# Kernel optimization log

Measured on AMD Instinct MI355X. Metric: run time of the kernel, lower is better.

## Reference

```python
import jax, jax.numpy as jnp
import numpy as np
from jax import lax

GUARD_CELLS = 80
BG_CELLS = 80
ALPHA = 1.8
CFAR_UNITS = 1 + 2 * GUARD_CELLS + 2 * BG_CELLS          # 321
GUARD_UNITS = 2 * GUARD_CELLS + 1                         # 161
BG_AREA = CFAR_UNITS ** 2 - GUARD_UNITS ** 2              # background ring cell count
FRONT_DIV = (GUARD_UNITS ** 2) * ALPHA


def box_sum(x, k):
    """Same-padded KxK box sum over NCHW x (C=1), via separable 1D convs.

    Mathematically identical to a Conv2d with all-ones KxK kernel, zero bias,
    padding (k-1)//2 -- but O(N*K) instead of O(N*K^2).
    """
    p = (k - 1) // 2
    kh = jnp.ones((1, 1, k, 1), x.dtype)  # OIHW
    kw = jnp.ones((1, 1, 1, k), x.dtype)
    y = lax.conv_general_dilated(x, kh, window_strides=(1, 1), padding=[(p, p), (0, 0)])
    y = lax.conv_general_dilated(y, kw, window_strides=(1, 1), padding=[(0, 0), (p, p)])
    return y


def setup_inputs() -> dict:
    key = jax.random.key(0)
    x = jax.random.uniform(key, (4, 1, 1024, 1024), dtype=jnp.float32)
    return {"x": x}


def reference(x) -> jnp.ndarray:
    allsum = box_sum(x, CFAR_UNITS)            # conv1: 321x321 ones box
    front = box_sum(x, GUARD_UNITS)            # conv2: 161x161 ones box
    back = (allsum - front) / jnp.float32(BG_AREA)     # div1: 1x1 conv = scale
    front = front / jnp.float32(FRONT_DIV)             # div2: 1x1 conv = scale
    return front / back
```

## Files before the change

kernel.cpp:

```cpp
#include <hip/hip_runtime.h>
#include <hip/hip_bf16.h>


#define IMG 4
#define H 1024
#define W 1024
#define SEGR 4
#define NSEG 256
#define PADL 164
#define PADR 164
#define ROWLEN (PADL + W + PADR)

__global__ __launch_bounds__(256) void hbv_kernel(const float* __restrict__ x,
                                                  float* __restrict__ g161,
                                                  float* __restrict__ g321,
                                                  float* __restrict__ Btot) {
    __shared__ float P[4][ROWLEN];
    const int wave = threadIdx.x >> 6;
    const int lane = threadIdx.x & 63;
    const int tid  = threadIdx.x;
    const int blk  = blockIdx.x;
    const size_t rowbase = (size_t)blk << 2;

    {
        const size_t row = rowbase + wave;
        const float4* xr = reinterpret_cast<const float4*>(x + row * W);
        float v[16];
        float4 a0 = xr[(lane << 2) + 0];
        float4 a1 = xr[(lane << 2) + 1];
        float4 a2 = xr[(lane << 2) + 2];
        float4 a3 = xr[(lane << 2) + 3];
        v[0]=a0.x; v[1]=a0.y; v[2]=a0.z; v[3]=a0.w;
        v[4]=a1.x; v[5]=a1.y; v[6]=a1.z; v[7]=a1.w;
        v[8]=a2.x; v[9]=a2.y; v[10]=a2.z; v[11]=a2.w;
        v[12]=a3.x; v[13]=a3.y; v[14]=a3.z; v[15]=a3.w;
        float s = 0.f;
#pragma unroll
        for (int j = 0; j < 16; ++j) { s += v[j]; v[j] = s; }
        float t = s;
#pragma unroll
        for (int d = 1; d < 64; d <<= 1) {
            float u = __shfl_up(t, d, 64);
            if (lane >= d) t += u;
        }
        const float off = t - s;
#pragma unroll
        for (int j = 0; j < 16; ++j) v[j] += off;
        const float tot = __shfl(t, 63, 64);

        float* rowP = P[wave];
        float4* Pr = reinterpret_cast<float4*>(rowP + PADL);
        Pr[(lane << 2) + 0] = make_float4(v[0], v[1], v[2], v[3]);
        Pr[(lane << 2) + 1] = make_float4(v[4], v[5], v[6], v[7]);
        Pr[(lane << 2) + 2] = make_float4(v[8], v[9], v[10], v[11]);
        Pr[(lane << 2) + 3] = make_float4(v[12], v[13], v[14], v[15]);
        float4* Pz = reinterpret_cast<float4*>(rowP);
        if (lane < 41) {
            Pz[lane]       = make_float4(0.f, 0.f, 0.f, 0.f);
            Pz[297 + lane] = make_float4(tot, tot, tot, tot);
        }
    }
    __syncthreads();

    float acc1[4] = {0.f, 0.f, 0.f, 0.f};
    float acc3[4] = {0.f, 0.f, 0.f, 0.f};
#pragma unroll
    for (int rr = 0; rr < SEGR; ++rr) {
        const float* Pr = &P[rr][PADL];
        float* o1 = g161 + (rowbase + rr) * W;
        float* o3 = g321 + (rowbase + rr) * W;
#pragma unroll
        for (int j = 0; j < 4; ++j) {
            const int c = tid + (j << 8);
            acc1[j] += Pr[c + 80]  - Pr[c - 81];
            acc3[j] += Pr[c + 160] - Pr[c - 161];
            o1[c] = acc1[j];
            o3[c] = acc3[j];
        }
    }

    const int img = blk >> 8;
    const int seg = blk & 255;
    float* bt1 = Btot + ((size_t)img << 18)         + ((size_t)seg << 10);
    float* bt3 = Btot + ((size_t)(IMG + img) << 18) + ((size_t)seg << 10);
#pragma unroll
    for (int j = 0; j < 4; ++j) {
        bt1[tid + (j << 8)] = acc1[j];
        bt3[tid + (j << 8)] = acc3[j];
    }
}

__global__ __launch_bounds__(256) void segscan_kernel(float* __restrict__ Btot) {
    __shared__ float T[4][64];
    const int wave = threadIdx.x >> 6;
    const int lane = threadIdx.x & 63;
    const int bi   = blockIdx.x >> 4;
    const int col  = ((blockIdx.x & 15) << 6) + lane;
    const size_t base = ((size_t)bi << 18) + ((size_t)(wave << 6) << 10) + col;

    float v[64];
#pragma unroll
    for (int s = 0; s < 64; ++s) v[s] = Btot[base + ((size_t)s << 10)];
    float run = 0.f;
#pragma unroll
    for (int s = 0; s < 64; ++s) { const float t = v[s]; v[s] = run; run += t; }
    T[wave][lane] = run;
    __syncthreads();
    float off = 0.f;
    for (int w = 0; w < wave; ++w) off += T[w][lane];
#pragma unroll
    for (int s = 0; s < 64; ++s) Btot[base + ((size_t)s << 10)] = v[s] + off;
}

__global__ __launch_bounds__(512) void final_kernel(const float* __restrict__ g161,
                                                    const float* __restrict__ g321,
                                                    const float* __restrict__ SP,
                                                    float* __restrict__ out) {
    const int img = blockIdx.x >> 9;
    const int r   = ((blockIdx.x & 511) << 1) + (threadIdx.x >> 8);
    const int c4  = threadIdx.x & 255;

    const float4* P1 = reinterpret_cast<const float4*>(g161 + ((size_t)img << 20));
    const float4* P3 = reinterpret_cast<const float4*>(g321 + ((size_t)img << 20));
    const float4* SP1 = reinterpret_cast<const float4*>(SP) + ((size_t)img << 16);
    const float4* SP3 = reinterpret_cast<const float4*>(SP) + ((size_t)(IMG + img) << 16);

    const int hi1 = min(r + 80, H - 1),  lo1 = r - 81;
    const int hi3 = min(r + 160, H - 1), lo3 = r - 161;

    float4 f  = P1[((size_t)hi1 << 8) + c4];
    float4 fs = SP1[(((size_t)hi1 >> 2) << 8) + c4];
    float fx = f.x + fs.x, fy = f.y + fs.y, fz = f.z + fs.z, fw = f.w + fs.w;
    if (lo1 >= 0) {
        float4 g  = P1[((size_t)lo1 << 8) + c4];
        float4 gs = SP1[(((size_t)lo1 >> 2) << 8) + c4];
        fx -= g.x + gs.x; fy -= g.y + gs.y; fz -= g.z + gs.z; fw -= g.w + gs.w;
    }
    float4 a  = P3[((size_t)hi3 << 8) + c4];
    float4 as = SP3[(((size_t)hi3 >> 2) << 8) + c4];
    float ax = a.x + as.x, ay = a.y + as.y, az = a.z + as.z, aw = a.w + as.w;
    if (lo3 >= 0) {
        float4 g  = P3[((size_t)lo3 << 8) + c4];
        float4 gs = SP3[(((size_t)lo3 >> 2) << 8) + c4];
        ax -= g.x + gs.x; ay -= g.y + gs.y; az -= g.z + gs.z; aw -= g.w + gs.w;
    }

    const float SCALE = (float)(77120.0 / 46657.8);
    float4 o;
    o.x = SCALE * fx * __builtin_amdgcn_rcpf(ax - fx);
    o.y = SCALE * fy * __builtin_amdgcn_rcpf(ay - fy);
    o.z = SCALE * fz * __builtin_amdgcn_rcpf(az - fz);
    o.w = SCALE * fw * __builtin_amdgcn_rcpf(aw - fw);
    reinterpret_cast<float4*>(out + ((size_t)img << 20) + ((size_t)r << 10))[c4] = o;
}

extern "C" void kernel_launch(void* const* d_in, const int* in_sizes, int n_in,
                              void* d_out, int out_size, void* d_ws, size_t ws_size,
                              hipStream_t stream) {
    const float* x = (const float*)d_in[0];
    float* outp = (float*)d_out;
    float* g161 = (float*)d_ws;
    float* g321 = g161 + (size_t)IMG * H * W;
    float* Btot = g321 + (size_t)IMG * H * W;

    hbv_kernel<<<dim3(IMG * NSEG), dim3(256), 0, stream>>>(x, g161, g321, Btot);
    segscan_kernel<<<dim3(128), dim3(256), 0, stream>>>(Btot);
    final_kernel<<<dim3(IMG * (H / 2)), dim3(512), 0, stream>>>(g161, g321, Btot, outp);
}
```

Baseline: 91.61 us.

## Use a single 2D summed-area table instead of two horizontal box-sum planes

The first kernel now writes one summed-area table of row prefix sums accumulated within 4-row segments, where it previously wrote separate 161- and 321-wide horizontal box-sum planes. The segment scan takes the last row of each segment from that table and stores per-segment prefix offsets separately. The final kernel rebuilds both box sums from the table by staging the needed corner rows in shared memory and doing horizontal lookups. This halves the intermediate plane written and read through global memory. In exchange it adds shared-memory staging, extra syncs, and a different ordering of floating-point sums, so precision can differ from the previous version.

```diff
diff --git a/kernel.cpp b/kernel.cpp
--- a/kernel.cpp
+++ b/kernel.cpp
@@ -7,24 +7,17 @@
 #define W 1024
 #define SEGR 4
 #define NSEG 256
-#define PADL 164
-#define PADR 164
-#define ROWLEN (PADL + W + PADR)
 
-__global__ __launch_bounds__(256) void hbv_kernel(const float* __restrict__ x,
-                                                  float* __restrict__ g161,
-                                                  float* __restrict__ g321,
-                                                  float* __restrict__ Btot) {
-    __shared__ float P[4][ROWLEN];
+__global__ __launch_bounds__(256) void sat_kernel(const float* __restrict__ x,
+                                                  float* __restrict__ Q) {
+    __shared__ float P[4][W];
     const int wave = threadIdx.x >> 6;
     const int lane = threadIdx.x & 63;
     const int tid  = threadIdx.x;
-    const int blk  = blockIdx.x;
-    const size_t rowbase = (size_t)blk << 2;
+    const size_t rowbase = (size_t)blockIdx.x << 2;
 
     {
-        const size_t row = rowbase + wave;
-        const float4* xr = reinterpret_cast<const float4*>(x + row * W);
+        const float4* xr = reinterpret_cast<const float4*>(x + (rowbase + wave) * W);
         float v[16];
         float4 a0 = xr[(lane << 2) + 0];
         float4 a1 = xr[(lane << 2) + 1];
@@ -46,61 +39,40 @@
         const float off = t - s;
 #pragma unroll
         for (int j = 0; j < 16; ++j) v[j] += off;
-        const float tot = __shfl(t, 63, 64);
 
-        float* rowP = P[wave];
-        float4* Pr = reinterpret_cast<float4*>(rowP + PADL);
+        float4* Pr = reinterpret_cast<float4*>(P[wave]);
         Pr[(lane << 2) + 0] = make_float4(v[0], v[1], v[2], v[3]);
         Pr[(lane << 2) + 1] = make_float4(v[4], v[5], v[6], v[7]);
         Pr[(lane << 2) + 2] = make_float4(v[8], v[9], v[10], v[11]);
         Pr[(lane << 2) + 3] = make_float4(v[12], v[13], v[14], v[15]);
-        float4* Pz = reinterpret_cast<float4*>(rowP);
-        if (lane < 41) {
-            Pz[lane]       = make_float4(0.f, 0.f, 0.f, 0.f);
-            Pz[297 + lane] = make_float4(tot, tot, tot, tot);
-        }
     }
     __syncthreads();
 
-    float acc1[4] = {0.f, 0.f, 0.f, 0.f};
-    float acc3[4] = {0.f, 0.f, 0.f, 0.f};
+    float4 acc = make_float4(0.f, 0.f, 0.f, 0.f);
+    float4* Qo = reinterpret_cast<float4*>(Q) + (rowbase << 8) + tid;
 #pragma unroll
     for (int rr = 0; rr < SEGR; ++rr) {
-        const float* Pr = &P[rr][PADL];
-        float* o1 = g161 + (rowbase + rr) * W;
-        float* o3 = g321 + (rowbase + rr) * W;
-#pragma unroll
-        for (int j = 0; j < 4; ++j) {
-            const int c = tid + (j << 8);
-            acc1[j] += Pr[c + 80]  - Pr[c - 81];
-            acc3[j] += Pr[c + 160] - Pr[c - 161];
-            o1[c] = acc1[j];
-            o3[c] = acc3[j];
-        }
-    }
-
-    const int img = blk >> 8;
-    const int seg = blk & 255;
-    float* bt1 = Btot + ((size_t)img << 18)         + ((size_t)seg << 10);
-    float* bt3 = Btot + ((size_t)(IMG + img) << 18) + ((size_t)seg << 10);
-#pragma unroll
-    for (int j = 0; j < 4; ++j) {
-        bt1[tid + (j << 8)] = acc1[j];
-        bt3[tid + (j << 8)] = acc3[j];
+        const float4 h = reinterpret_cast<const float4*>(P[rr])[tid];
+        acc.x += h.x; acc.y += h.y; acc.z += h.z; acc.w += h.w;
+        Qo[(size_t)rr << 8] = acc;
     }
 }
 
-__global__ __launch_bounds__(256) void segscan_kernel(float* __restrict__ Btot) {
+__global__ __launch_bounds__(256) void segscan_kernel(const float* __restrict__ Q,
+                                                      float* __restrict__ SP) {
     __shared__ float T[4][64];
     const int wave = threadIdx.x >> 6;
     const int lane = threadIdx.x & 63;
-    const int bi   = blockIdx.x >> 4;
+    const int img  = blockIdx.x >> 4;
     const int col  = ((blockIdx.x & 15) << 6) + lane;
-    const size_t base = ((size_t)bi << 18) + ((size_t)(wave << 6) << 10) + col;
 
+    const float* Qi = Q + ((size_t)img << 20);
     float v[64];
 #pragma unroll
-    for (int s = 0; s < 64; ++s) v[s] = Btot[base + ((size_t)s << 10)];
+    for (int s = 0; s < 64; ++s) {
+        const int seg = (wave << 6) + s;
+        v[s] = Qi[((size_t)((seg << 2) + 3) << 10) + col];
+    }
     float run = 0.f;
 #pragma unroll
     for (int s = 0; s < 64; ++s) { const float t = v[s]; v[s] = run; run += t; }
@@ -108,50 +80,98 @@
     __syncthreads();
     float off = 0.f;
     for (int w = 0; w < wave; ++w) off += T[w][lane];
+    float* SPo = SP + ((size_t)img << 18) + col;
 #pragma unroll
-    for (int s = 0; s < 64; ++s) Btot[base + ((size_t)s << 10)] = v[s] + off;
+    for (int s = 0; s < 64; ++s)
+        SPo[(size_t)(((wave << 6) + s)) << 10] = v[s] + off;
 }
 
-__global__ __launch_bounds__(512) void final_kernel(const float* __restrict__ g161,
-                                                    const float* __restrict__ g321,
+__global__ __launch_bounds__(256) void final_kernel(const float* __restrict__ Q,
                                                     const float* __restrict__ SP,
                                                     float* __restrict__ out) {
-    const int img = blockIdx.x >> 9;
-    const int r   = ((blockIdx.x & 511) << 1) + (threadIdx.x >> 8);
-    const int c4  = threadIdx.x & 255;
+    __shared__ float S[8][W];
+    const int tid = threadIdx.x;
+    const int img = blockIdx.x >> 8;
+    const int r0  = (blockIdx.x & 255) << 2;
 
-    const float4* P1 = reinterpret_cast<const float4*>(g161 + ((size_t)img << 20));
-    const float4* P3 = reinterpret_cast<const float4*>(g321 + ((size_t)img << 20));
-    const float4* SP1 = reinterpret_cast<const float4*>(SP) + ((size_t)img << 16);
-    const float4* SP3 = reinterpret_cast<const float4*>(SP) + ((size_t)(IMG + img) << 16);
+    const float4* Q4  = reinterpret_cast<const float4*>(Q)  + ((size_t)img << 18);
+    const float4* SP4 = reinterpret_cast<const float4*>(SP) + ((size_t)img << 16);
+    float4* S4 = reinterpret_cast<float4*>(&S[0][0]);
 
-    const int hi1 = min(r + 80, H - 1),  lo1 = r - 81;
-    const int hi3 = min(r + 160, H - 1), lo3 = r - 161;
+#pragma unroll
+    for (int i = 0; i < 4; ++i) {
+        {
+            const int row = min(r0 + 80 + i, H - 1);
+            const float4 a = Q4[((size_t)row << 8) + tid];
+            const float4 b = SP4[((size_t)(row >> 2) << 8) + tid];
+            S4[(i << 8) + tid] = make_float4(a.x + b.x, a.y + b.y, a.z + b.z, a.w + b.w);
+        }
+        {
+            const int row = r0 - 81 + i;
+            float4 vv = make_float4(0.f, 0.f, 0.f, 0.f);
+            if (row >= 0) {
+                const float4 a = Q4[((size_t)row << 8) + tid];
+                const float4 b = SP4[((size_t)(row >> 2) << 8) + tid];
+                vv = make_float4(a.x + b.x, a.y + b.y, a.z + b.z, a.w + b.w);
+            }
+            S4[((4 + i) << 8) + tid] = vv;
+        }
+    }
+    __syncthreads();
 
-    float4 f  = P1[((size_t)hi1 << 8) + c4];
-    float4 fs = SP1[(((size_t)hi1 >> 2) << 8) + c4];
-    float fx = f.x + fs.x, fy = f.y + fs.y, fz = f.z + fs.z, fw = f.w + fs.w;
-    if (lo1 >= 0) {
-        float4 g  = P1[((size_t)lo1 << 8) + c4];
-        float4 gs = SP1[(((size_t)lo1 >> 2) << 8) + c4];
-        fx -= g.x + gs.x; fy -= g.y + gs.y; fz -= g.z + gs.z; fw -= g.w + gs.w;
+    float fr[4][4];
+#pragma unroll
+    for (int i = 0; i < 4; ++i) {
+#pragma unroll
+        for (int j = 0; j < 4; ++j) {
+            const int c  = tid + (j << 8);
+            const int kp = min(c + 80, W - 1);
+            const int km = c - 81;
+            const float m = (km >= 0) ? 1.f : 0.f;
+            const int k  = max(km, 0);
+            fr[i][j] = (S[i][kp] - m * S[i][k]) - (S[4 + i][kp] - m * S[4 + i][k]);
+        }
     }
-    float4 a  = P3[((size_t)hi3 << 8) + c4];
-    float4 as = SP3[(((size_t)hi3 >> 2) << 8) + c4];
-    float ax = a.x + as.x, ay = a.y + as.y, az = a.z + as.z, aw = a.w + as.w;
-    if (lo3 >= 0) {
-        float4 g  = P3[((size_t)lo3 << 8) + c4];
-        float4 gs = SP3[(((size_t)lo3 >> 2) << 8) + c4];
-        ax -= g.x + gs.x; ay -= g.y + gs.y; az -= g.z + gs.z; aw -= g.w + gs.w;
+    __syncthreads();
+
+#pragma unroll
+    for (int i = 0; i < 4; ++i) {
+        {
+            const int row = min(r0 + 160 + i, H - 1);
+            const float4 a = Q4[((size_t)row << 8) + tid];
+            const float4 b = SP4[((size_t)(row >> 2) << 8) + tid];
+            S4[(i << 8) + tid] = make_float4(a.x + b.x, a.y + b.y, a.z + b.z, a.w + b.w);
+        }
+        {
+            const int row = r0 - 161 + i;
+            float4 vv = make_float4(0.f, 0.f, 0.f, 0.f);
+            if (row >= 0) {
+                const float4 a = Q4[((size_t)row << 8) + tid];
+                const float4 b = SP4[((size_t)(row >> 2) << 8) + tid];
+                vv = make_float4(a.x + b.x, a.y + b.y, a.z + b.z, a.w + b.w);
+            }
+            S4[((4 + i) << 8) + tid] = vv;
+        }
     }
+    __syncthreads();
 
     const float SCALE = (float)(77120.0 / 46657.8);
-    float4 o;
-    o.x = SCALE * fx * __builtin_amdgcn_rcpf(ax - fx);
-    o.y = SCALE * fy * __builtin_amdgcn_rcpf(ay - fy);
-    o.z = SCALE * fz * __builtin_amdgcn_rcpf(az - fz);
-    o.w = SCALE * fw * __builtin_amdgcn_rcpf(aw - fw);
-    reinterpret_cast<float4*>(out + ((size_t)img << 20) + ((size_t)r << 10))[c4] = o;
+    float* o = out + ((size_t)img << 20);
+#pragma unroll
+    for (int i = 0; i < 4; ++i) {
+        const int r = r0 + i;
+#pragma unroll
+        for (int j = 0; j < 4; ++j) {
+            const int c  = tid + (j << 8);
+            const int kp = min(c + 160, W - 1);
+            const int km = c - 161;
+            const float m = (km >= 0) ? 1.f : 0.f;
+            const int k  = max(km, 0);
+            const float allsum = (S[i][kp] - m * S[i][k]) - (S[4 + i][kp] - m * S[4 + i][k]);
+            const float front  = fr[i][j];
+            o[((size_t)r << 10) + c] = SCALE * front * __builtin_amdgcn_rcpf(allsum - front);
+        }
+    }
 }
 
 extern "C" void kernel_launch(void* const* d_in, const int* in_sizes, int n_in,
@@ -159,11 +179,10 @@
                               hipStream_t stream) {
     const float* x = (const float*)d_in[0];
     float* outp = (float*)d_out;
-    float* g161 = (float*)d_ws;
-    float* g321 = g161 + (size_t)IMG * H * W;
-    float* Btot = g321 + (size_t)IMG * H * W;
+    float* Q   = (float*)d_ws;
+    float* SPb = Q + (size_t)IMG * H * W;
 
-    hbv_kernel<<<dim3(IMG * NSEG), dim3(256), 0, stream>>>(x, g161, g321, Btot);
-    segscan_kernel<<<dim3(128), dim3(256), 0, stream>>>(Btot);
-    final_kernel<<<dim3(IMG * (H / 2)), dim3(512), 0, stream>>>(g161, g321, Btot, outp);
+    sat_kernel<<<dim3(IMG * NSEG), dim3(256), 0, stream>>>(x, Q);
+    segscan_kernel<<<dim3(64), dim3(256), 0, stream>>>(Q, SPb);
+    final_kernel<<<dim3(IMG * (H / 4)), dim3(256), 0, stream>>>(Q, SPb, outp);
 }
```

New measurement: 85.98 us. 6.2% less time.
